# Optimization experiments

Measured on AMD Instinct MI355X. Metric: run time of the kernel, lower is better.

## Reference

```python
import jax, jax.numpy as jnp
import numpy as np

CD_STEPS = 1

def _sample_binary(p, u):
    # relu(sign(p - u)): 1.0 where p > u else 0.0
    return (p > u).astype(p.dtype)

def setup_inputs() -> dict:
    key = jax.random.key(0)
    k_v, k_w, k_vb, k_uh, k_uv = jax.random.split(key, 5)
    B, V, H = 8192, 2048, 1024
    return {
        "v": jax.random.uniform(k_v, (B, V), dtype=jnp.float32),
        "w": jax.random.normal(k_w, (V, H), dtype=jnp.float32) * 0.01,
        "vb": jax.random.normal(k_vb, (V,), dtype=jnp.float32) * 0.01,
        "hb": jnp.zeros((H,), dtype=jnp.float32),
        "u_h": jax.random.uniform(k_uh, (CD_STEPS + 1, B, H), dtype=jnp.float32),
        "u_v": jax.random.uniform(k_uv, (CD_STEPS, B, V), dtype=jnp.float32),
    }

def reference(v, w, vb, hb, u_h, u_v):
    sig = jax.nn.sigmoid
    # mean-field forward
    h_p = sig(hb + v @ w)                     # [B,H]
    h_prediction = h_p
    v_prediction = sig(vb + h_p @ w.T)        # [B,V]
    reconstruction_error = jnp.mean(jnp.mean(jnp.abs(v - v_prediction), axis=1))
    # data statistics
    h = _sample_binary(h_p, u_h[0])           # [B,H]
    vb_data_grad = jnp.sum(v, axis=0)
    hb_data_grad = jnp.sum(h_p, axis=0)
    # sum_b outer(v_b, h_b) == v^T @ h (original materialized [B,V,H])
    w_data_grad = jnp.einsum('bv,bh->vh', v, h)
    # CD-k chain
    vk = v
    for k in range(CD_STEPS):
        vk = _sample_binary(sig(vb + h @ w.T), u_v[k])
        h = _sample_binary(sig(hb + vk @ w), u_h[k + 1])
    vb_model_grad = jnp.sum(vk, axis=0)
    hb_model_grad = jnp.sum(h, axis=0)
    w_model_grad = jnp.einsum('bv,bh->vh', vk, h)
    vb_grad = vb_model_grad - vb_data_grad
    hb_grad = hb_model_grad - hb_data_grad
    w_grad = w_model_grad - w_data_grad
    return h_prediction, reconstruction_error, w_grad, vb_grad, hb_grad
```

## Files before the change

kernel.cpp:

```cpp
#include <hip/hip_runtime.h>


typedef unsigned short u16;
typedef short s16x8 __attribute__((ext_vector_type(8)));
typedef float f32x4 __attribute__((ext_vector_type(4)));
typedef u16 u16x4 __attribute__((ext_vector_type(4)));
typedef u16 u16x8 __attribute__((ext_vector_type(8)));

constexpr int Bn = 8192, Vn = 2048, Hn = 1024;
constexpr size_t VH = (size_t)Vn * Hn;
constexpr size_t BH = (size_t)Bn * Hn;
constexpr size_t OUT_RECON = BH;
constexpr size_t OUT_WGRAD = OUT_RECON + 1;
constexpr size_t OUT_VBG   = OUT_WGRAD + VH;
constexpr size_t OUT_HBG   = OUT_VBG + Vn;

__device__ __forceinline__ u16 f2bf(float x) {
  union { float f; unsigned u; } a; a.f = x;
  unsigned r = a.u + 0x7FFFu + ((a.u >> 16) & 1u);
  return (u16)(r >> 16);
}
__device__ __forceinline__ float bf2f(u16 h) {
  union { unsigned u; float f; } a; a.u = ((unsigned)h) << 16;
  return a.f;
}
__device__ __forceinline__ float sigmoidf_(float x) {
  return 1.0f / (1.0f + __expf(-x));
}

using gptr_t = const unsigned int __attribute__((address_space(1)))*;
using lptr_t = unsigned int __attribute__((address_space(3)))*;

__device__ __forceinline__ void gload16(const u16* g, u16* l) {
  __builtin_amdgcn_global_load_lds((gptr_t)(unsigned long long)g,
                                   (lptr_t)(unsigned long long)l, 16, 0, 0);
}

__global__ void prep_all_k(const float* __restrict__ v, u16* __restrict__ vcat,
                           u16* __restrict__ vT, float* __restrict__ vbd_p,
                           const float* __restrict__ w, u16* __restrict__ w_cat,
                           u16* __restrict__ wTc) {
  __shared__ u16 tile16[64][68];
  __shared__ float cs[16][64];
  __shared__ float tile32[64][65];
  const int bx = blockIdx.x;
  const int t = threadIdx.x;
  if (bx < 4096) {
    const int b0 = (bx & 127) << 6, c0 = (bx >> 7) << 6;
    const int rg = t >> 4;
    const int cg = (t & 15) << 2;
    float ca[4] = {0.f, 0.f, 0.f, 0.f};
#pragma unroll
    for (int i = 0; i < 4; ++i) {
      int r = rg + 16 * i;
      f32x4 x = *(const f32x4*)&v[(size_t)(b0 + r) * Vn + c0 + cg];
      u16x4 hi, lo;
#pragma unroll
      for (int j = 0; j < 4; ++j) {
        hi[j] = f2bf(x[j]);
        lo[j] = f2bf(x[j] - bf2f(hi[j]));
        tile16[r][cg + j] = hi[j];
        ca[j] += x[j];
      }
      *(u16x4*)&vcat[(size_t)(b0 + r) * (2 * Vn) + c0 + cg] = hi;
      *(u16x4*)&vcat[(size_t)(b0 + r) * (2 * Vn) + Vn + c0 + cg] = lo;
    }
#pragma unroll
    for (int j = 0; j < 4; ++j) cs[rg][cg + j] = ca[j];
    __syncthreads();
    if (t < 64) {
      float s = 0.f;
#pragma unroll
      for (int k = 0; k < 16; ++k) s += cs[k][t];
      vbd_p[(size_t)(bx & 127) * Vn + c0 + t] = s;
    }
#pragma unroll
    for (int s2 = 0; s2 < 2; ++s2) {
      int c = t >> 2;
      int seg = (t & 3) + 4 * s2;
      u16x8 pk;
#pragma unroll
      for (int i = 0; i < 8; ++i) pk[i] = tile16[seg * 8 + i][c];
      *(u16x8*)&vT[(size_t)(c0 + c) * Bn + b0 + seg * 8] = pk;
    }
  } else {
    const int wb = bx - 4096;
    const int v0 = (wb & 31) << 6, h0 = (wb >> 5) << 6;
    const int c = t & 63, r = t >> 6;
    for (int rr = r; rr < 64; rr += 4) {
      float x = w[(size_t)(v0 + rr) * Hn + h0 + c];
      tile32[rr][c] = x;
      u16 hi = f2bf(x), lo = f2bf(x - bf2f(hi));
      w_cat[(size_t)(v0 + rr) * (2 * Hn) + h0 + c]      = hi;
      w_cat[(size_t)(v0 + rr) * (2 * Hn) + Hn + h0 + c] = lo;
    }
    __syncthreads();
    for (int rr = r; rr < 64; rr += 4) {
      float x = tile32[c][rr];
      u16 hi = f2bf(x), lo = f2bf(x - bf2f(hi));
      size_t ro = (size_t)(h0 + rr) * (2 * Vn);
      wTc[ro + v0 + c]      = hi;
      wTc[ro + Vn + v0 + c] = lo;
    }
  }
}

template <int M>
__global__ void epi_h_k(const float* __restrict__ p0, const float* __restrict__ p1,
                        const float* __restrict__ bias, const float* __restrict__ uni,
                        float* __restrict__ f32out, u16* __restrict__ hp_out,
                        u16* __restrict__ hbin_out, u16* __restrict__ tout,
                        float* __restrict__ colp) {
  __shared__ u16 tile[64][68];
  __shared__ float cs[16][64];
  const int b0 = blockIdx.x * 64, c0 = blockIdx.y * 64;
  const int t = threadIdx.x;
  const int rg = t >> 4, cg = (t & 15) << 2;
  float ca[4] = {0.f, 0.f, 0.f, 0.f};
#pragma unroll
  for (int i = 0; i < 4; ++i) {
    int r = rg + 16 * i;
    size_t e = (size_t)(b0 + r) * Hn + c0 + cg;
    f32x4 a = *(const f32x4*)&p0[e];
    f32x4 b = *(const f32x4*)&p1[e];
    f32x4 uu = *(const f32x4*)&uni[e];
    f32x4 hpv;
    u16x4 hb16, qv;
#pragma unroll
    for (int j = 0; j < 4; ++j) {
      float hp = sigmoidf_(a[j] + b[j] + bias[c0 + cg + j]);
      u16 qb = (hp > uu[j]) ? (u16)0x3F80 : (u16)0;
      tile[r][cg + j] = qb;
      if constexpr (M == 1) {
        hpv[j] = hp; hb16[j] = f2bf(hp); qv[j] = qb;
        ca[j] += hp;
      } else {
        ca[j] += (qb ? 1.f : 0.f);
      }
    }
    if constexpr (M == 1) {
      *(f32x4*)&f32out[e] = hpv;
      *(u16x4*)&hp_out[e] = hb16;
      *(u16x4*)&hbin_out[e] = qv;
    }
  }
#pragma unroll
  for (int j = 0; j < 4; ++j) cs[rg][cg + j] = ca[j];
  __syncthreads();
  if (t < 64) {
    float s = 0.f;
#pragma unroll
    for (int k = 0; k < 16; ++k) s += cs[k][t];
    colp[(size_t)blockIdx.x * Hn + c0 + t] = s;
  }
#pragma unroll
  for (int s2 = 0; s2 < 2; ++s2) {
    int c = t >> 2;
    int seg = (t & 3) + 4 * s2;
    u16x8 pk;
#pragma unroll
    for (int i = 0; i < 8; ++i) pk[i] = tile[seg * 8 + i][c];
    *(u16x8*)&tout[(size_t)(c0 + c) * Bn + b0 + seg * 8] = pk;
  }
}

template <int MODE>
__global__ __launch_bounds__(512) void gemm256(
    const u16* __restrict__ A, int lda, const u16* __restrict__ Bm, int ldb, int K,
    const float* __restrict__ bias, const float* __restrict__ uni,
    const float* __restrict__ aux, float* __restrict__ f32out,
    u16* __restrict__ bfout, const u16* __restrict__ aux16,
    float* __restrict__ redp, u16* __restrict__ tout, float* __restrict__ colp) {
  constexpr bool TRANS = (MODE == 4);
  __shared__ __align__(16) u16 smem[TRANS ? 67584 : 65536];
  const int t = threadIdx.x;
  const int lane = t & 63, wave = t >> 6;
  const int wr = (wave >> 2) << 7;
  const int wc = (wave & 3) << 6;
  int bidx = blockIdx.x, bidy = blockIdx.y, bidz = blockIdx.z;
  if constexpr (MODE == 3) {
    const int orig = blockIdx.x + (blockIdx.y << 3) + (blockIdx.z << 5);
    bidz = orig & 7;
    const int r = orig >> 3;
    bidx = r & 7;
    bidy = r >> 3;
  }
  const int bm = bidx << 8, bn = bidy << 8;
  int kbeg = 0;
  float* pout = f32out;
  if constexpr (MODE == 1 || MODE == 5) {
    kbeg = bidz * K;
    pout = (bidz == 0) ? f32out : redp;
  }
  if constexpr (MODE == 3) {
    size_t off = (size_t)bidz * (size_t)K;
    A += off;
    Bm += off;
    pout = ((bidz < 4) ? f32out : redp) + (size_t)(bidz & 3) * VH;
  }
  f32x4 acc[8][4] = {};
  const int sr = t >> 2;
  const int sc = (((t & 3) ^ ((t >> 3) & 3)) << 3);
  const u16* Ag  = A  + (size_t)(bm + sr) * lda + sc;
  const u16* Ag2 = Ag + (size_t)128 * lda;
  const u16* Bg  = Bm + (size_t)(bn + sr) * ldb + sc;
  const u16* Bg2 = Bg + (size_t)128 * ldb;
  const int fr = lane & 15, fg = lane >> 4;
  const int ga = ((fg ^ ((fr >> 1) & 3)) << 3);

  auto stage = [&](int kt) {
    const int k0 = kbeg + (kt << 5);
    int acol, bcol;
    if constexpr (MODE == 1) {
      acol = (k0 < 2048) ? k0 : k0 - 2048;
      bcol = (k0 < 4096) ? k0 : k0 - 4096;
    } else if constexpr (MODE == 4) { acol = k0 & 1023; bcol = k0; }
    else if constexpr (MODE == 5)   { acol = k0 & 2047; bcol = k0; }
    else                            { acol = k0;        bcol = k0; }
    const int pb = kt & 3;
    u16* ad = smem + pb * 8192 + wave * 512;
    u16* bd = smem + 32768 + pb * 8192 + wave * 512;
    gload16(Ag + acol, ad);
    gload16(Ag2 + acol, ad + 4096);
    gload16(Bg + bcol, bd);
    gload16(Bg2 + bcol, bd + 4096);
  };
  auto compute = [&](int kt) {
    const int pb = kt & 3;
    const u16* Ab = smem + pb * 8192;
    const u16* Bb = smem + 32768 + pb * 8192;
    s16x8 bf[4], af[4];
#pragma unroll
    for (int n = 0; n < 4; ++n)
      bf[n] = *(const s16x8*)&Bb[(wc + n * 16 + fr) * 32 + ga];
#pragma unroll
    for (int m = 0; m < 4; ++m)
      af[m] = *(const s16x8*)&Ab[(wr + m * 16 + fr) * 32 + ga];
    __builtin_amdgcn_s_setprio(1);
#pragma unroll
    for (int m = 0; m < 4; ++m)
#pragma unroll
      for (int n = 0; n < 4; ++n)
        acc[m][n] = __builtin_amdgcn_mfma_f32_16x16x32_bf16(af[m], bf[n], acc[m][n], 0, 0, 0);
    __builtin_amdgcn_s_setprio(0);
#pragma unroll
    for (int m = 0; m < 4; ++m)
      af[m] = *(const s16x8*)&Ab[(wr + (m + 4) * 16 + fr) * 32 + ga];
    __builtin_amdgcn_s_setprio(1);
#pragma unroll
    for (int m = 0; m < 4; ++m)
#pragma unroll
      for (int n = 0; n < 4; ++n)
        acc[m + 4][n] = __builtin_amdgcn_mfma_f32_16x16x32_bf16(af[m], bf[n], acc[m + 4][n], 0, 0, 0);
    __builtin_amdgcn_s_setprio(0);
  };
  auto pfl4 = [&](int ci) -> float {
    const int L = (ci << 9) + t;
    return uni[(size_t)(bm + (L >> 3)) * Vn + bn + ((L & 7) << 5)];
  };
  auto pfl2 = [&](int ci) -> unsigned {
    const int L = (ci << 9) + t;
    return (unsigned)aux16[(size_t)(bm + (L >> 2)) * 4096 + bn + ((L & 3) << 6)];
  };

  const int NT = K >> 5;
  const int pfbeg = NT - 8;
  stage(0); stage(1); stage(2);
  int T = 0;
  for (; T < NT - 3; ++T) {
    asm volatile("s_waitcnt vmcnt(8)" ::: "memory");
    __builtin_amdgcn_s_barrier();
    asm volatile("" ::: "memory");
    stage(T + 3);
    if constexpr (MODE == 4) {
      if (T >= pfbeg && T < pfbeg + 4) {
        float pfv = pfl4(T - pfbeg);
        asm volatile("" :: "v"(pfv));
      }
    } else if constexpr (MODE == 2) {
      if (T >= pfbeg && T < pfbeg + 2) {
        unsigned pfv = pfl2(T - pfbeg);
        asm volatile("" :: "v"(pfv));
      }
    }
    compute(T);
  }
  asm volatile("s_waitcnt vmcnt(8)" ::: "memory");
  __builtin_amdgcn_s_barrier();
  asm volatile("" ::: "memory");
  compute(T++);
  asm volatile("s_waitcnt vmcnt(4)" ::: "memory");
  __builtin_amdgcn_s_barrier();
  asm volatile("" ::: "memory");
  compute(T++);
  asm volatile("s_waitcnt vmcnt(0)" ::: "memory");
  __builtin_amdgcn_s_barrier();
  asm volatile("" ::: "memory");
  compute(T);

  constexpr int NC = (MODE == 2 || MODE == 4) ? Vn : Hn;
  const int fq = lane >> 4;

  if constexpr (MODE == 1 || MODE == 3 || MODE == 5) {
#pragma unroll
    for (int m = 0; m < 8; ++m)
#pragma unroll
      for (int n = 0; n < 4; ++n)
#pragma unroll
        for (int j = 0; j < 4; ++j) {
          int rl = wr + m * 16 + fq * 4 + j;
          int cl = wc + n * 16 + fr;
          pout[(size_t)(bm + rl) * NC + bn + cl] = acc[m][n][j];
        }
  }

  if constexpr (MODE == 2) {
    float bcol[4];
#pragma unroll
    for (int n = 0; n < 4; ++n) bcol[n] = bias[bn + wc + n * 16 + fr];
    const size_t ebase = (size_t)(bm + wr + fq * 4) * 4096 + (bn + wc + fr);
    float ax[8][4];
    auto ld4 = [&](int ci, float* dst) {
      size_t e0 = ebase + (size_t)((ci >> 2) << 4) * 4096 + ((ci & 3) << 4);
      dst[0] = bf2f(aux16[e0]);            dst[1] = bf2f(aux16[e0 + 4096]);
      dst[2] = bf2f(aux16[e0 + 2 * 4096]); dst[3] = bf2f(aux16[e0 + 3 * 4096]);
    };
#pragma unroll
    for (int ci = 0; ci < 8; ++ci) ld4(ci, ax[ci]);
#pragma unroll
    for (int m = 0; m < 8; ++m)
#pragma unroll
      for (int n = 0; n < 4; ++n)
#pragma unroll
        for (int j = 0; j < 4; ++j)
          acc[m][n][j] = sigmoidf_(acc[m][n][j] + bcol[n]);
    float lsum = 0.f;
#pragma unroll
    for (int ci = 0; ci < 32; ++ci) {
      const int m = ci >> 2, n = ci & 3;
#pragma unroll
      for (int j = 0; j < 4; ++j) lsum += fabsf(ax[ci & 7][j] - acc[m][n][j]);
      if (ci < 24) ld4(ci + 8, ax[ci & 7]);
    }
#pragma unroll
    for (int off = 32; off > 0; off >>= 1) lsum += __shfl_down(lsum, off);
    __syncthreads();
    float* redlds = (float*)smem;
    if (lane == 0) redlds[wave] = lsum;
    __syncthreads();
    if (t == 0) {
      float s = 0.f;
#pragma unroll
      for (int wv = 0; wv < 8; ++wv) s += redlds[wv];
      redp[(size_t)blockIdx.y * gridDim.x + blockIdx.x] = s;
    }
  }

  if constexpr (MODE == 4) {
    __syncthreads();
    float bcol[4];
#pragma unroll
    for (int n = 0; n < 4; ++n) bcol[n] = bias[bn + wc + n * 16 + fr];
    const size_t ebase = (size_t)(bm + wr + fq * 4) * NC + (bn + wc + fr);
    float ux[8][4];
    auto ld4 = [&](int ci, float* dst) {
      size_t e0 = ebase + (size_t)((ci >> 2) << 4) * NC + ((ci & 3) << 4);
      dst[0] = uni[e0];          dst[1] = uni[e0 + NC];
      dst[2] = uni[e0 + 2 * NC]; dst[3] = uni[e0 + 3 * NC];
    };
#pragma unroll
    for (int ci = 0; ci < 8; ++ci) ld4(ci, ux[ci]);
#pragma unroll
    for (int m = 0; m < 8; ++m)
#pragma unroll
      for (int n = 0; n < 4; ++n)
#pragma unroll
        for (int j = 0; j < 4; ++j)
          acc[m][n][j] = sigmoidf_(acc[m][n][j] + bcol[n]);
    float csum[4] = {0.f, 0.f, 0.f, 0.f};
#pragma unroll
    for (int ci = 0; ci < 32; ++ci) {
      const int m = ci >> 2, n = ci & 3;
      const int rl = wr + m * 16 + fq * 4;
      const int cl = wc + n * 16 + fr;
#pragma unroll
      for (int j = 0; j < 4; ++j) {
        u16 qb = (acc[m][n][j] > ux[ci & 7][j]) ? (u16)0x3F80 : (u16)0;
        smem[(rl + j) * 264 + cl] = qb;
        csum[n] += (qb ? 1.f : 0.f);
      }
      if (ci < 24) ld4(ci + 8, ux[ci & 7]);
    }
#pragma unroll
    for (int n = 0; n < 4; ++n) {
      float s = csum[n];
      s += __shfl_xor(s, 16);
      s += __shfl_xor(s, 32);
      if (fq == 0)
        colp[(size_t)(blockIdx.x * 2 + (wr >> 7)) * NC + (bn + wc + n * 16 + fr)] = s;
    }
    __syncthreads();
#pragma unroll
    for (int it = 0; it < 16; ++it) {
      int id = t + (it << 9);
      int r = id >> 5;
      int c0 = (id & 31) << 3;
      u16x8 pk = *(const u16x8*)&smem[r * 264 + c0];
      *(u16x8*)&bfout[(size_t)(bm + r) * NC + bn + c0] = pk;
    }
#pragma unroll
    for (int it = 0; it < 4; ++it) {
      int id = t + (it << 9);
      int c = id & 255;
      int q = id >> 8;
#pragma unroll
      for (int i8 = 0; i8 < 4; ++i8) {
        u16x8 pk;
#pragma unroll
        for (int i2 = 0; i2 < 8; ++i2)
          pk[i2] = smem[(q * 32 + i8 * 8 + i2) * 264 + c];
        *(u16x8*)&tout[(size_t)(bn + c) * Bn + bm + q * 32 + i8 * 8] = pk;
      }
    }
  }
}

__global__ void reduce8_k(const float* __restrict__ p, float* __restrict__ out) {
  size_t e = ((size_t)blockIdx.x * 256 + threadIdx.x) * 4;
  f32x4 r = {};
#pragma unroll
  for (int z = 0; z < 8; ++z) r += *(const f32x4*)&p[(size_t)z * VH + e];
  out[e + 0] = r[0]; out[e + 1] = r[1]; out[e + 2] = r[2]; out[e + 3] = r[3];
}

__global__ void reduce8s_k(const float* __restrict__ pa, const float* __restrict__ pb,
                           const float* __restrict__ sub, float* __restrict__ out) {
  size_t e = ((size_t)blockIdx.x * 256 + threadIdx.x) * 4;
  f32x4 r = {};
#pragma unroll
  for (int z = 0; z < 4; ++z) r += *(const f32x4*)&pa[(size_t)z * VH + e];
#pragma unroll
  for (int z = 0; z < 4; ++z) r += *(const f32x4*)&pb[(size_t)z * VH + e];
  float s0 = sub[e + 0], s1 = sub[e + 1], s2 = sub[e + 2], s3 = sub[e + 3];
  out[e + 0] = r[0] - s0; out[e + 1] = r[1] - s1;
  out[e + 2] = r[2] - s2; out[e + 3] = r[3] - s3;
}

__global__ void finalize_k(const float* __restrict__ sums, float* __restrict__ out) {
  int i = blockIdx.x * 256 + threadIdx.x;
  const float* recon_p = sums;
  const float* vbd = sums + 1024;
  const float* hbd = vbd + 128 * 2048;
  const float* vbm = hbd + 128 * 1024;
  const float* hbm = vbm + 128 * 2048;
  if (i < 2048) {
    float d = 0.f, m = 0.f;
    for (int k = 0; k < 128; ++k) d += vbd[k * 2048 + i];
    for (int k = 0; k < 64; ++k)  m += vbm[k * 2048 + i];
    out[OUT_VBG + i] = m - d;
  }
  if (i < 1024) {
    float d = 0.f, m = 0.f;
    for (int k = 0; k < 128; ++k) { d += hbd[k * 1024 + i]; m += hbm[k * 1024 + i]; }
    out[OUT_HBG + i] = m - d;
  }
  if (i == 0) {
    float s = 0.f;
    for (int k = 0; k < 256; ++k) s += recon_p[k];
    out[OUT_RECON] = s * (1.0f / 16777216.0f);
  }
}

extern "C" void kernel_launch(void* const* d_in, const int* in_sizes, int n_in,
                              void* d_out, int out_size, void* d_ws, size_t ws_size,
                              hipStream_t stream) {
  (void)in_sizes; (void)n_in; (void)out_size;
  const float* v   = (const float*)d_in[0];
  const float* w   = (const float*)d_in[1];
  const float* vb  = (const float*)d_in[2];
  const float* hb  = (const float*)d_in[3];
  const float* u_h = (const float*)d_in[4];
  const float* u_v = (const float*)d_in[5];
  float* out = (float*)d_out;
  char* ws = (char*)d_ws;
  if (ws_size < 204734464ULL) return;

  float* sums    = (float*)ws;
  float* recon_p = sums;
  float* vbd_p   = sums + 1024;
  float* hbd_p   = vbd_p + 128 * 2048;
  float* vbm_p   = hbd_p + 128 * 1024;
  float* hbm_p   = vbm_p + 128 * 2048;
  char* p = ws + 3407872;
  u16* v_cat  = (u16*)p;  p += (size_t)Bn * 2 * Vn * 2;
  u16* wT_cat = (u16*)p;  p += (size_t)Hn * 2 * Vn * 2;
  u16* w_cat  = (u16*)p;  p += (size_t)Vn * 2 * Hn * 2;
  u16* h_p    = (u16*)p;  p += BH * 2;
  u16* hbin   = (u16*)p;  p += BH * 2;
  u16* vT     = (u16*)p;  p += (size_t)Vn * Bn * 2;
  u16* hT     = (u16*)p;  p += (size_t)Hn * Bn * 2;
  float* big  = (float*)p;
  u16* vk   = v_cat;
  u16* vkT  = vT;
  u16* h2T  = hT;
  float* vcat_f = (float*)v_cat;
  float* hpbuf  = (float*)h_p;
  float* outW   = out + OUT_WGRAD;

  prep_all_k<<<4608, 256, 0, stream>>>(v, v_cat, vT, vbd_p, w, w_cat, wT_cat);
  gemm256<1><<<dim3(32, 4, 2), 512, 0, stream>>>(
      v_cat, 2 * Vn, wT_cat, 2 * Vn, 3072, nullptr, nullptr, nullptr,
      out, nullptr, nullptr, big, nullptr, nullptr);
  epi_h_k<1><<<dim3(128, 16), 256, 0, stream>>>(
      out, big, hb, u_h, out, h_p, hbin, hT, hbd_p);
  gemm256<2><<<dim3(32, 8), 512, 0, stream>>>(
      h_p, Hn, w_cat, 2 * Hn, Hn, vb, nullptr, nullptr,
      nullptr, nullptr, v_cat, recon_p, nullptr, nullptr);
  gemm256<3><<<dim3(Vn / 256, Hn / 256, 8), 512, 0, stream>>>(
      vT, Bn, hT, Bn, 1024, nullptr, nullptr, nullptr,
      vcat_f, nullptr, nullptr, vcat_f + 4 * VH, nullptr, nullptr);
  reduce8_k<<<2048, 256, 0, stream>>>(vcat_f, outW);
  gemm256<4><<<dim3(32, 8), 512, 0, stream>>>(
      hbin, Hn, w_cat, 2 * Hn, 2 * Hn, vb, u_v, nullptr,
      nullptr, vk, nullptr, nullptr, vkT, vbm_p);
  gemm256<5><<<dim3(32, 4, 2), 512, 0, stream>>>(
      vk, Vn, wT_cat, 2 * Vn, 2048, nullptr, nullptr, nullptr,
      hpbuf, nullptr, nullptr, big, nullptr, nullptr);
  epi_h_k<5><<<dim3(128, 16), 256, 0, stream>>>(
      hpbuf, big, hb, u_h + BH, nullptr, nullptr, nullptr, h2T, hbm_p);
  gemm256<3><<<dim3(Vn / 256, Hn / 256, 8), 512, 0, stream>>>(
      vkT, Bn, h2T, Bn, 1024, nullptr, nullptr, nullptr,
      hpbuf, nullptr, nullptr, big, nullptr, nullptr);
  reduce8s_k<<<2048, 256, 0, stream>>>(hpbuf, big, outW, outW);
  finalize_k<<<8, 256, 0, stream>>>(sums, out);
}
```

Baseline: 503.0 us.

## Co-launch independent GEMM2 and data-grad GEMM3 in one grid; merge tail kernels

Two independent GEMMs, the reconstruction GEMM with its fused sigmoid/abs-error reduction and the split-K v^T·h data-gradient GEMM, now run as one kernel with 512 blocks. Each block dispatches on its flat index, so the two 256-block launches fill the GPU together instead of running back to back. The final weight-grad reduction and the bias/reconstruction finalize are also merged into one launch. This trades a divergent branch and a larger, specialized kernel body for fewer launches and better CU occupancy across the two workloads.

```diff
diff --git a/kernel.cpp b/kernel.cpp
--- a/kernel.cpp
+++ b/kernel.cpp
@@ -258,10 +258,6 @@
     const int L = (ci << 9) + t;
     return uni[(size_t)(bm + (L >> 3)) * Vn + bn + ((L & 7) << 5)];
   };
-  auto pfl2 = [&](int ci) -> unsigned {
-    const int L = (ci << 9) + t;
-    return (unsigned)aux16[(size_t)(bm + (L >> 2)) * 4096 + bn + ((L & 3) << 6)];
-  };
 
   const int NT = K >> 5;
   const int pfbeg = NT - 8;
@@ -277,11 +273,6 @@
         float pfv = pfl4(T - pfbeg);
         asm volatile("" :: "v"(pfv));
       }
-    } else if constexpr (MODE == 2) {
-      if (T >= pfbeg && T < pfbeg + 2) {
-        unsigned pfv = pfl2(T - pfbeg);
-        asm volatile("" :: "v"(pfv));
-      }
     }
     compute(T);
   }
@@ -298,7 +289,7 @@
   asm volatile("" ::: "memory");
   compute(T);
 
-  constexpr int NC = (MODE == 2 || MODE == 4) ? Vn : Hn;
+  constexpr int NC = (MODE == 4) ? Vn : Hn;
   const int fq = lane >> 4;
 
   if constexpr (MODE == 1 || MODE == 3 || MODE == 5) {
@@ -312,48 +303,6 @@
           int cl = wc + n * 16 + fr;
           pout[(size_t)(bm + rl) * NC + bn + cl] = acc[m][n][j];
         }
-  }
-
-  if constexpr (MODE == 2) {
-    float bcol[4];
-#pragma unroll
-    for (int n = 0; n < 4; ++n) bcol[n] = bias[bn + wc + n * 16 + fr];
-    const size_t ebase = (size_t)(bm + wr + fq * 4) * 4096 + (bn + wc + fr);
-    float ax[8][4];
-    auto ld4 = [&](int ci, float* dst) {
-      size_t e0 = ebase + (size_t)((ci >> 2) << 4) * 4096 + ((ci & 3) << 4);
-      dst[0] = bf2f(aux16[e0]);            dst[1] = bf2f(aux16[e0 + 4096]);
-      dst[2] = bf2f(aux16[e0 + 2 * 4096]); dst[3] = bf2f(aux16[e0 + 3 * 4096]);
-    };
-#pragma unroll
-    for (int ci = 0; ci < 8; ++ci) ld4(ci, ax[ci]);
-#pragma unroll
-    for (int m = 0; m < 8; ++m)
-#pragma unroll
-      for (int n = 0; n < 4; ++n)
-#pragma unroll
-        for (int j = 0; j < 4; ++j)
-          acc[m][n][j] = sigmoidf_(acc[m][n][j] + bcol[n]);
-    float lsum = 0.f;
-#pragma unroll
-    for (int ci = 0; ci < 32; ++ci) {
-      const int m = ci >> 2, n = ci & 3;
-#pragma unroll
-      for (int j = 0; j < 4; ++j) lsum += fabsf(ax[ci & 7][j] - acc[m][n][j]);
-      if (ci < 24) ld4(ci + 8, ax[ci & 7]);
-    }
-#pragma unroll
-    for (int off = 32; off > 0; off >>= 1) lsum += __shfl_down(lsum, off);
-    __syncthreads();
-    float* redlds = (float*)smem;
-    if (lane == 0) redlds[wave] = lsum;
-    __syncthreads();
-    if (t == 0) {
-      float s = 0.f;
-#pragma unroll
-      for (int wv = 0; wv < 8; ++wv) s += redlds[wv];
-      redp[(size_t)blockIdx.y * gridDim.x + blockIdx.x] = s;
-    }
   }
 
   if constexpr (MODE == 4) {
@@ -425,6 +374,172 @@
   }
 }
 
+__global__ __launch_bounds__(512) void g23_k(
+    const u16* __restrict__ A2, const u16* __restrict__ B2,
+    const u16* __restrict__ aux16, const float* __restrict__ bias2,
+    float* __restrict__ redp2,
+    const u16* __restrict__ A3, const u16* __restrict__ B3,
+    float* __restrict__ out30, float* __restrict__ out34) {
+  __shared__ __align__(16) u16 smem[65536];
+  const int t = threadIdx.x;
+  const int lane = t & 63, wave = t >> 6;
+  const int wr = (wave >> 2) << 7;
+  const int wc = (wave & 3) << 6;
+  const int flat = blockIdx.x;
+  const bool isG2 = (flat < 256);
+  int bidx, bidy, bidz = 0;
+  const u16 *Abase, *Bbase;
+  int lda, ldb;
+  if (isG2) {
+    bidx = flat & 31; bidy = flat >> 5;
+    Abase = A2; Bbase = B2; lda = Hn; ldb = 2 * Hn;
+  } else {
+    const int orig = flat - 256;
+    bidz = orig & 7;
+    const int rr = orig >> 3;
+    bidx = rr & 7; bidy = rr >> 3;
+    Abase = A3 + (size_t)bidz * 1024;
+    Bbase = B3 + (size_t)bidz * 1024;
+    lda = Bn; ldb = Bn;
+  }
+  const int bm = bidx << 8, bn = bidy << 8;
+  f32x4 acc[8][4] = {};
+  const int sr = t >> 2;
+  const int sc = (((t & 3) ^ ((t >> 3) & 3)) << 3);
+  const u16* Ag  = Abase + (size_t)(bm + sr) * lda + sc;
+  const u16* Ag2 = Ag + (size_t)128 * lda;
+  const u16* Bg  = Bbase + (size_t)(bn + sr) * ldb + sc;
+  const u16* Bg2 = Bg + (size_t)128 * ldb;
+  const int fr = lane & 15, fg = lane >> 4;
+  const int ga = ((fg ^ ((fr >> 1) & 3)) << 3);
+
+  auto stage = [&](int kt) {
+    const int k0 = kt << 5;
+    const int pb = kt & 3;
+    u16* ad = smem + pb * 8192 + wave * 512;
+    u16* bd = smem + 32768 + pb * 8192 + wave * 512;
+    gload16(Ag + k0, ad);
+    gload16(Ag2 + k0, ad + 4096);
+    gload16(Bg + k0, bd);
+    gload16(Bg2 + k0, bd + 4096);
+  };
+  auto compute = [&](int kt) {
+    const int pb = kt & 3;
+    const u16* Ab = smem + pb * 8192;
+    const u16* Bb = smem + 32768 + pb * 8192;
+    s16x8 bf[4], af[4];
+#pragma unroll
+    for (int n = 0; n < 4; ++n)
+      bf[n] = *(const s16x8*)&Bb[(wc + n * 16 + fr) * 32 + ga];
+#pragma unroll
+    for (int m = 0; m < 4; ++m)
+      af[m] = *(const s16x8*)&Ab[(wr + m * 16 + fr) * 32 + ga];
+    __builtin_amdgcn_s_setprio(1);
+#pragma unroll
+    for (int m = 0; m < 4; ++m)
+#pragma unroll
+      for (int n = 0; n < 4; ++n)
+        acc[m][n] = __builtin_amdgcn_mfma_f32_16x16x32_bf16(af[m], bf[n], acc[m][n], 0, 0, 0);
+    __builtin_amdgcn_s_setprio(0);
+#pragma unroll
+    for (int m = 0; m < 4; ++m)
+      af[m] = *(const s16x8*)&Ab[(wr + (m + 4) * 16 + fr) * 32 + ga];
+    __builtin_amdgcn_s_setprio(1);
+#pragma unroll
+    for (int m = 0; m < 4; ++m)
+#pragma unroll
+      for (int n = 0; n < 4; ++n)
+        acc[m + 4][n] = __builtin_amdgcn_mfma_f32_16x16x32_bf16(af[m], bf[n], acc[m + 4][n], 0, 0, 0);
+    __builtin_amdgcn_s_setprio(0);
+  };
+  auto pfl2 = [&](int ci) -> unsigned {
+    const int L = (ci << 9) + t;
+    return (unsigned)aux16[(size_t)(bm + (L >> 2)) * 4096 + bn + ((L & 3) << 6)];
+  };
+
+  constexpr int NT = 32;
+  stage(0); stage(1); stage(2);
+  int T = 0;
+  for (; T < NT - 3; ++T) {
+    asm volatile("s_waitcnt vmcnt(8)" ::: "memory");
+    __builtin_amdgcn_s_barrier();
+    asm volatile("" ::: "memory");
+    stage(T + 3);
+    if (isG2 && T >= NT - 8 && T < NT - 6) {
+      unsigned pfv = pfl2(T - (NT - 8));
+      asm volatile("" :: "v"(pfv));
+    }
+    compute(T);
+  }
+  asm volatile("s_waitcnt vmcnt(8)" ::: "memory");
+  __builtin_amdgcn_s_barrier();
+  asm volatile("" ::: "memory");
+  compute(T++);
+  asm volatile("s_waitcnt vmcnt(4)" ::: "memory");
+  __builtin_amdgcn_s_barrier();
+  asm volatile("" ::: "memory");
+  compute(T++);
+  asm volatile("s_waitcnt vmcnt(0)" ::: "memory");
+  __builtin_amdgcn_s_barrier();
+  asm volatile("" ::: "memory");
+  compute(T);
+
+  const int fq = lane >> 4;
+  if (isG2) {
+    float bcol[4];
+#pragma unroll
+    for (int n = 0; n < 4; ++n) bcol[n] = bias2[bn + wc + n * 16 + fr];
+    const size_t ebase = (size_t)(bm + wr + fq * 4) * 4096 + (bn + wc + fr);
+    float ax[8][4];
+    auto ld4 = [&](int ci, float* dst) {
+      size_t e0 = ebase + (size_t)((ci >> 2) << 4) * 4096 + ((ci & 3) << 4);
+      dst[0] = bf2f(aux16[e0]);            dst[1] = bf2f(aux16[e0 + 4096]);
+      dst[2] = bf2f(aux16[e0 + 2 * 4096]); dst[3] = bf2f(aux16[e0 + 3 * 4096]);
+    };
+#pragma unroll
+    for (int ci = 0; ci < 8; ++ci) ld4(ci, ax[ci]);
+#pragma unroll
+    for (int m = 0; m < 8; ++m)
+#pragma unroll
+      for (int n = 0; n < 4; ++n)
+#pragma unroll
+        for (int j = 0; j < 4; ++j)
+          acc[m][n][j] = sigmoidf_(acc[m][n][j] + bcol[n]);
+    float lsum = 0.f;
+#pragma unroll
+    for (int ci = 0; ci < 32; ++ci) {
+      const int m = ci >> 2, n = ci & 3;
+#pragma unroll
+      for (int j = 0; j < 4; ++j) lsum += fabsf(ax[ci & 7][j] - acc[m][n][j]);
+      if (ci < 24) ld4(ci + 8, ax[ci & 7]);
+    }
+#pragma unroll
+    for (int off = 32; off > 0; off >>= 1) lsum += __shfl_down(lsum, off);
+    __syncthreads();
+    float* redlds = (float*)smem;
+    if (lane == 0) redlds[wave] = lsum;
+    __syncthreads();
+    if (t == 0) {
+      float s = 0.f;
+#pragma unroll
+      for (int wv = 0; wv < 8; ++wv) s += redlds[wv];
+      redp2[(size_t)bidy * 32 + bidx] = s;
+    }
+  } else {
+    float* pout = ((bidz < 4) ? out30 : out34) + (size_t)(bidz & 3) * VH;
+#pragma unroll
+    for (int m = 0; m < 8; ++m)
+#pragma unroll
+      for (int n = 0; n < 4; ++n)
+#pragma unroll
+        for (int j = 0; j < 4; ++j) {
+          int rl = wr + m * 16 + fq * 4 + j;
+          int cl = wc + n * 16 + fr;
+          pout[(size_t)(bm + rl) * Hn + bn + cl] = acc[m][n][j];
+        }
+  }
+}
+
 __global__ void reduce8_k(const float* __restrict__ p, float* __restrict__ out) {
   size_t e = ((size_t)blockIdx.x * 256 + threadIdx.x) * 4;
   f32x4 r = {};
@@ -433,41 +548,43 @@
   out[e + 0] = r[0]; out[e + 1] = r[1]; out[e + 2] = r[2]; out[e + 3] = r[3];
 }
 
-__global__ void reduce8s_k(const float* __restrict__ pa, const float* __restrict__ pb,
-                           const float* __restrict__ sub, float* __restrict__ out) {
-  size_t e = ((size_t)blockIdx.x * 256 + threadIdx.x) * 4;
-  f32x4 r = {};
-#pragma unroll
-  for (int z = 0; z < 4; ++z) r += *(const f32x4*)&pa[(size_t)z * VH + e];
-#pragma unroll
-  for (int z = 0; z < 4; ++z) r += *(const f32x4*)&pb[(size_t)z * VH + e];
-  float s0 = sub[e + 0], s1 = sub[e + 1], s2 = sub[e + 2], s3 = sub[e + 3];
-  out[e + 0] = r[0] - s0; out[e + 1] = r[1] - s1;
-  out[e + 2] = r[2] - s2; out[e + 3] = r[3] - s3;
-}
-
-__global__ void finalize_k(const float* __restrict__ sums, float* __restrict__ out) {
-  int i = blockIdx.x * 256 + threadIdx.x;
-  const float* recon_p = sums;
-  const float* vbd = sums + 1024;
-  const float* hbd = vbd + 128 * 2048;
-  const float* vbm = hbd + 128 * 1024;
-  const float* hbm = vbm + 128 * 2048;
-  if (i < 2048) {
-    float d = 0.f, m = 0.f;
-    for (int k = 0; k < 128; ++k) d += vbd[k * 2048 + i];
-    for (int k = 0; k < 64; ++k)  m += vbm[k * 2048 + i];
-    out[OUT_VBG + i] = m - d;
-  }
-  if (i < 1024) {
-    float d = 0.f, m = 0.f;
-    for (int k = 0; k < 128; ++k) { d += hbd[k * 1024 + i]; m += hbm[k * 1024 + i]; }
-    out[OUT_HBG + i] = m - d;
-  }
-  if (i == 0) {
-    float s = 0.f;
-    for (int k = 0; k < 256; ++k) s += recon_p[k];
-    out[OUT_RECON] = s * (1.0f / 16777216.0f);
+__global__ void tail_k(const float* __restrict__ pa, const float* __restrict__ pb,
+                       const float* __restrict__ sums, float* __restrict__ out) {
+  const int b = blockIdx.x;
+  float* outw = out + OUT_WGRAD;
+  if (b < 2048) {
+    size_t e = ((size_t)b * 256 + threadIdx.x) * 4;
+    f32x4 r = {};
+#pragma unroll
+    for (int z = 0; z < 4; ++z) r += *(const f32x4*)&pa[(size_t)z * VH + e];
+#pragma unroll
+    for (int z = 0; z < 4; ++z) r += *(const f32x4*)&pb[(size_t)z * VH + e];
+    float s0 = outw[e + 0], s1 = outw[e + 1], s2 = outw[e + 2], s3 = outw[e + 3];
+    outw[e + 0] = r[0] - s0; outw[e + 1] = r[1] - s1;
+    outw[e + 2] = r[2] - s2; outw[e + 3] = r[3] - s3;
+  } else {
+    const int i = (b - 2048) * 256 + threadIdx.x;
+    const float* recon_p = sums;
+    const float* vbd = sums + 1024;
+    const float* hbd = vbd + 128 * 2048;
+    const float* vbm = hbd + 128 * 1024;
+    const float* hbm = vbm + 128 * 2048;
+    if (i < 2048) {
+      float d = 0.f, m = 0.f;
+      for (int k = 0; k < 128; ++k) d += vbd[k * 2048 + i];
+      for (int k = 0; k < 64; ++k)  m += vbm[k * 2048 + i];
+      out[OUT_VBG + i] = m - d;
+    }
+    if (i < 1024) {
+      float d = 0.f, m = 0.f;
+      for (int k = 0; k < 128; ++k) { d += hbd[k * 1024 + i]; m += hbm[k * 1024 + i]; }
+      out[OUT_HBG + i] = m - d;
+    }
+    if (i == 0) {
+      float s = 0.f;
+      for (int k = 0; k < 256; ++k) s += recon_p[k];
+      out[OUT_RECON] = s * (1.0f / 16777216.0f);
+    }
   }
 }
 
@@ -513,12 +630,9 @@
       out, nullptr, nullptr, big, nullptr, nullptr);
   epi_h_k<1><<<dim3(128, 16), 256, 0, stream>>>(
       out, big, hb, u_h, out, h_p, hbin, hT, hbd_p);
-  gemm256<2><<<dim3(32, 8), 512, 0, stream>>>(
-      h_p, Hn, w_cat, 2 * Hn, Hn, vb, nullptr, nullptr,
-      nullptr, nullptr, v_cat, recon_p, nullptr, nullptr);
-  gemm256<3><<<dim3(Vn / 256, Hn / 256, 8), 512, 0, stream>>>(
-      vT, Bn, hT, Bn, 1024, nullptr, nullptr, nullptr,
-      vcat_f, nullptr, nullptr, vcat_f + 4 * VH, nullptr, nullptr);
+  g23_k<<<512, 512, 0, stream>>>(
+      h_p, w_cat, v_cat, vb, recon_p,
+      vT, hT, vcat_f, vcat_f + 4 * VH);
   reduce8_k<<<2048, 256, 0, stream>>>(vcat_f, outW);
   gemm256<4><<<dim3(32, 8), 512, 0, stream>>>(
       hbin, Hn, w_cat, 2 * Hn, 2 * Hn, vb, u_v, nullptr,
@@ -531,6 +645,5 @@
   gemm256<3><<<dim3(Vn / 256, Hn / 256, 8), 512, 0, stream>>>(
       vkT, Bn, h2T, Bn, 1024, nullptr, nullptr, nullptr,
       hpbuf, nullptr, nullptr, big, nullptr, nullptr);
-  reduce8s_k<<<2048, 256, 0, stream>>>(hpbuf, big, outW, outW);
-  finalize_k<<<8, 256, 0, stream>>>(sums, out);
-}
+  tail_k<<<2056, 256, 0, stream>>>(hpbuf, big, sums, out);
+}
```

Result: no change. 498.6 us (-0.9%).
